# Kernel optimization log

Hardware: AMD Instinct MI355X
Metric: run time of the kernel (lower is better)

Reference implementation:

```python
import jax, jax.numpy as jnp
import numpy as np
from jax import lax

HIDDEN_CH = 32
KS = 3


def _conv(x, w):
    # x: [B, Cin, H, W], w: [Cout, Cin, k, k] -> [B, Cout, H, W] (SAME padding)
    return lax.conv_general_dilated(
        x, w, window_strides=(1, 1), padding='SAME',
        dimension_numbers=('NCHW', 'OIHW', 'NCHW'))


def _cell(x, h, gw, gb, cw, cb):
    combined = jnp.concatenate([x, h], axis=1)
    gates = jax.nn.sigmoid(_conv(combined, gw) + gb[None, :, None, None])
    r, z = jnp.split(gates, 2, axis=1)
    combined_r = jnp.concatenate([x, r * h], axis=1)
    n = jnp.tanh(_conv(combined_r, cw) + cb[None, :, None, None])
    return (1.0 - z) * h + z * n


def setup_inputs() -> dict:
    key = jax.random.key(0)
    ks = jax.random.split(key, 9)
    B, T, H, W = 8, 16, 128, 128
    hc = HIDDEN_CH
    seq = jax.random.normal(ks[0], (B, T, H, W), dtype=jnp.float32)

    def conv_init(k, cout, cin):
        fan_in = cin * KS * KS
        bound = 1.0 / np.sqrt(fan_in)
        return jax.random.uniform(k, (cout, cin, KS, KS), jnp.float32, -bound, bound)

    def bias_init(k, cout, cin):
        bound = 1.0 / np.sqrt(cin * KS * KS)
        return jax.random.uniform(k, (cout,), jnp.float32, -bound, bound)

    # Layer 0: input_ch=1, layer 1: input_ch=hc
    gw0 = conv_init(ks[1], 2 * hc, 1 + hc)
    gb0 = bias_init(ks[2], 2 * hc, 1 + hc)
    cw0 = conv_init(ks[3], hc, 1 + hc)
    cb0 = bias_init(ks[4], hc, 1 + hc)
    gw1 = conv_init(ks[5], 2 * hc, hc + hc)
    gb1 = bias_init(ks[6], 2 * hc, hc + hc)
    cw1 = conv_init(ks[7], hc, hc + hc)
    cb1 = bias_init(ks[8], hc, hc + hc)
    return {'seq': seq, 'gw0': gw0, 'gb0': gb0, 'cw0': cw0, 'cb0': cb0,
            'gw1': gw1, 'gb1': gb1, 'cw1': cw1, 'cb1': cb1}


def reference(seq, gw0, gb0, cw0, cb0, gw1, gb1, cw1, cb1):
    B, T, H, W = seq.shape
    hc = HIDDEN_CH
    h0 = jnp.zeros((B, hc, H, W), dtype=seq.dtype)
    h1 = jnp.zeros((B, hc, H, W), dtype=seq.dtype)
    # xs: [T, B, 1, H, W]
    xs = jnp.transpose(seq, (1, 0, 2, 3))[:, :, None, :, :]

    def step(carry, x_t):
        h0, h1 = carry
        h0 = _cell(x_t, h0, gw0, gb0, cw0, cb0)
        h1 = _cell(h0, h1, gw1, gb1, cw1, cb1)
        return (h0, h1), None

    (h0, h1), _ = lax.scan(step, (h0, h1), xs)
    return h1
```

## Files before the change

kernel.cpp:

```cpp
#include <hip/hip_runtime.h>


#define HH 128
#define PH 130
#define HW 16384
#define BB 8
#define TT 16

typedef _Float16 f16x8 __attribute__((ext_vector_type(8)));
typedef float f32x4 __attribute__((ext_vector_type(4)));
typedef unsigned int u32x4 __attribute__((ext_vector_type(4)));

__device__ __forceinline__ unsigned short f2h(float x){
    return __builtin_bit_cast(unsigned short, (_Float16)x);
}
__device__ __forceinline__ float h2f(unsigned short u){
    return (float)__builtin_bit_cast(_Float16, u);
}
__device__ __forceinline__ f16x8 ld_frag(const unsigned short* p){
    u32x4 v = *(const u32x4*)p;
    return __builtin_bit_cast(f16x8, v);
}
__device__ __forceinline__ f16x8 lds_frag_w(const unsigned short* base, int spix, int q){
    u32x4 v = *(const u32x4*)(base + spix * 32 + q * 8);
    return __builtin_bit_cast(f16x8, v);
}
__device__ __forceinline__ float sigmoid_f(float a){ return 1.0f / (1.0f + __expf(-a)); }
__device__ __forceinline__ float tanh_f(float a){ float e2 = __expf(2.0f * a); return 1.0f - 2.0f / (e2 + 1.0f); }

__device__ __forceinline__ void halo_rc(int s, int& gr, int& gc){
    s = s > 75 ? 75 : s;
    if (s < 34)      { gr = 0;            gc = s;      }
    else if (s < 68) { gr = 5;            gc = s - 34; }
    else if (s < 72) { gr = 1 + (s - 68); gc = 0;      }
    else             { gr = 1 + (s - 72); gc = 33;     }
}

__device__ __forceinline__ f16x8 x_im2col(const float* xt, int gr, int gc, int q){
    f16x8 v;
#pragma unroll
    for (int j = 0; j < 8; ++j) {
        int k = q * 8 + j;
        float f = 0.0f;
        if (k < 9) f = xt[(gr + k / 3) * 37 + gc + k % 3];
        v[j] = (_Float16)f;
    }
    return v;
}

__device__ __forceinline__ void stage_plane(unsigned short* slot,
    const unsigned short* __restrict__ g, int b, int prow0, int pcol0)
{
    const int wv = threadIdx.x >> 6, lane = threadIdx.x & 63;
    for (int k = wv; k < 18; k += 4) {
        int chunk = k * 64 + lane;
        int pix = chunk >> 2, part = chunk & 3;
        int r = pix / 36, c = pix - r * 36;
        int pr = prow0 + r; pr = pr < 0 ? 0 : (pr > 129 ? 129 : pr);
        int pc = pcol0 + c; pc = pc < 0 ? 0 : (pc > 129 ? 129 : pc);
        const unsigned short* ga = g + ((long)((b * PH + pr) * PH + pc) * 32 + part * 8);
        __builtin_amdgcn_global_load_lds(
            (const __attribute__((address_space(1))) unsigned int*)ga,
            (__attribute__((address_space(3))) unsigned int*)(slot + k * 512),
            16, 0, 0);
    }
}

__device__ __forceinline__ void stage_x(float* xt, const float* __restrict__ x,
                                        int irow0, int icol0)
{
    for (int p = threadIdx.x; p < 288; p += 256) {
        int r = p / 36, c = p - r * 36;
        int ir = irow0 + r, ic = icol0 + c;
        float v = 0.0f;
        if (ir >= 0 && ir < HH && ic >= 0 && ic < HH) v = x[ir * HH + ic];
        xt[r * 37 + c] = v;
    }
}

__global__ void prep_w(const float* __restrict__ w, unsigned short* __restrict__ wf,
                       int CO, int CIT, int NSTEP, int xmode)
{
    int idx = blockIdx.x * 256 + threadIdx.x;
    int total = NSTEP * CO * 32;
    if (idx >= total) return;
    int kk = idx & 31;
    int t  = idx >> 5;
    int co = t % CO;
    int s  = t / CO;
    float v = 0.0f;
    if (xmode && s == NSTEP - 1) {
        if (kk < 9) v = w[(co * CIT + 0) * 9 + kk];
    } else {
        int tap = s % 9;
        int cin = (s / 9) * 32 + kk + (xmode ? 1 : 0);
        v = w[(co * CIT + cin) * 9 + tap];
    }
    wf[idx] = f2h(v);
}

template<int L>
__global__ __launch_bounds__(256, (L == 0) ? 4 : 3)
void cell_fused(const unsigned short* __restrict__ Hin,
                unsigned short* __restrict__ Hout,
                const unsigned short* __restrict__ Xin,
                const float* __restrict__ xraw, long xbs,
                const unsigned short* __restrict__ Wg, const float* __restrict__ bg,
                const unsigned short* __restrict__ Wc, const float* __restrict__ bc)
{
    constexpr int NSLOT = (L == 0) ? 1 : 2;
    constexpr int KG = (L == 0) ? 10 : 18;
    constexpr int KC = (L == 0) ? 10 : 18;

    __shared__ __align__(16) unsigned short hsbuf[NSLOT][9216];
    __shared__ __align__(16) unsigned short rh[6528];
    __shared__ float xt[(L == 0) ? 296 : 1];

    unsigned short* hs0 = hsbuf[0];
    unsigned short* hs1 = hsbuf[NSLOT - 1];

    const int b  = blockIdx.y;
    const int tc = blockIdx.x & 3;
    const int tr = blockIdx.x >> 2;
    const int R0 = tr * 4, C0 = tc * 32;
    const int prow0 = R0 - 1, pcol0 = C0 - 1;

    if (L == 0) {
        stage_plane(hs0, Hin, b, prow0, pcol0);
        stage_x(xt, xraw + (long)b * xbs, R0 - 2, C0 - 2);
    } else {
        stage_plane(hs0, Xin, b, prow0, pcol0);
        stage_plane(hs1, Hin, b, prow0, pcol0);
    }
    __syncthreads();

    const int wv = threadIdx.x >> 6, lane = threadIdx.x & 63;
    const int m16 = lane & 15, q = lane >> 4;
    const unsigned short* hp = (L == 0) ? hs0 : hs1;

    int hr0, hc0, hr1, hc1;
    halo_rc(wv * 16 + m16, hr0, hc0);
    halo_rc(64 + m16, hr1, hc1);
    const bool HAS2 = (wv == 0);

    f32x4 gI[2][4];
    f32x4 gH[2][2];
#pragma unroll
    for (int ng = 0; ng < 4; ++ng) {
        float bv = bg[ng * 16 + m16];
#pragma unroll
        for (int mg = 0; mg < 2; ++mg) gI[mg][ng] = f32x4{bv, bv, bv, bv};
        if (ng < 2) { gH[0][ng] = f32x4{bv, bv, bv, bv}; gH[1][ng] = f32x4{bv, bv, bv, bv}; }
    }

#pragma unroll
    for (int s = 0; s < KG; ++s) {
        f16x8 Bf[4];
#pragma unroll
        for (int ng = 0; ng < 4; ++ng)
            Bf[ng] = ld_frag(Wg + (s * 64 + ng * 16 + m16) * 32 + q * 8);
        f16x8 AI[2], AH0, AH1;
        if (L == 0 && s == 9) {
#pragma unroll
            for (int mg = 0; mg < 2; ++mg)
                AI[mg] = x_im2col(xt, wv + 1, mg * 16 + 1 + m16, q);
            AH0 = x_im2col(xt, hr0, hc0, q);
            if (HAS2) AH1 = x_im2col(xt, hr1, hc1, q);
        } else {
            const int tap = (L == 0) ? s : (s % 9);
            const unsigned short* pl = (L == 1 && s >= 9) ? hs1 : hs0;
#pragma unroll
            for (int mg = 0; mg < 2; ++mg)
                AI[mg] = lds_frag_w(pl, (wv + 1 + tap / 3) * 36 + mg * 16 + 1 + m16 + tap % 3, q);
            AH0 = lds_frag_w(pl, (hr0 + tap / 3) * 36 + hc0 + tap % 3, q);
            if (HAS2) AH1 = lds_frag_w(pl, (hr1 + tap / 3) * 36 + hc1 + tap % 3, q);
        }
#pragma unroll
        for (int mg = 0; mg < 2; ++mg)
#pragma unroll
            for (int ng = 0; ng < 4; ++ng)
                gI[mg][ng] = __builtin_amdgcn_mfma_f32_16x16x32_f16(AI[mg], Bf[ng], gI[mg][ng], 0, 0, 0);
#pragma unroll
        for (int ng = 0; ng < 2; ++ng)
            gH[0][ng] = __builtin_amdgcn_mfma_f32_16x16x32_f16(AH0, Bf[ng], gH[0][ng], 0, 0, 0);
        if (HAS2) {
#pragma unroll
            for (int ng = 0; ng < 2; ++ng)
                gH[1][ng] = __builtin_amdgcn_mfma_f32_16x16x32_f16(AH1, Bf[ng], gH[1][ng], 0, 0, 0);
        }
    }

    unsigned int zpk[2][4];
#pragma unroll
    for (int mg = 0; mg < 2; ++mg)
#pragma unroll
        for (int rg = 0; rg < 4; ++rg) {
            int gr = wv + 1, gc = mg * 16 + 1 + q * 4 + rg;
            zpk[mg][rg] = (unsigned int)f2h(sigmoid_f(gI[mg][2][rg]))
                        | ((unsigned int)f2h(sigmoid_f(gI[mg][3][rg])) << 16);
#pragma unroll
            for (int ng = 0; ng < 2; ++ng) {
                int n = ng * 16 + m16;
                float rv = sigmoid_f(gI[mg][ng][rg]);
                float hv = h2f(hp[((gr + 1) * 36 + gc + 1) * 32 + n]);
                rh[(gr * 34 + gc) * 32 + n] = f2h(rv * hv);
            }
        }
#pragma unroll
    for (int rg = 0; rg < 4; ++rg) {
        int gr, gc; halo_rc(wv * 16 + q * 4 + rg, gr, gc);
#pragma unroll
        for (int ng = 0; ng < 2; ++ng) {
            int n = ng * 16 + m16;
            float rv = sigmoid_f(gH[0][ng][rg]);
            float hv = h2f(hp[((gr + 1) * 36 + gc + 1) * 32 + n]);
            rh[(gr * 34 + gc) * 32 + n] = f2h(rv * hv);
        }
    }
    if (HAS2) {
#pragma unroll
        for (int rg = 0; rg < 4; ++rg) {
            int gr, gc; halo_rc(64 + q * 4 + rg, gr, gc);
#pragma unroll
            for (int ng = 0; ng < 2; ++ng) {
                int n = ng * 16 + m16;
                float rv = sigmoid_f(gH[1][ng][rg]);
                float hv = h2f(hp[((gr + 1) * 36 + gc + 1) * 32 + n]);
                rh[(gr * 34 + gc) * 32 + n] = f2h(rv * hv);
            }
        }
    }
    __syncthreads();

    f32x4 cacc[2][2];
#pragma unroll
    for (int mg = 0; mg < 2; ++mg)
#pragma unroll
        for (int ng = 0; ng < 2; ++ng) {
            float bv = bc[ng * 16 + m16];
            cacc[mg][ng] = f32x4{bv, bv, bv, bv};
        }
#pragma unroll
    for (int s = 0; s < KC; ++s) {
        f16x8 Bf[2];
#pragma unroll
        for (int ng = 0; ng < 2; ++ng)
            Bf[ng] = ld_frag(Wc + (s * 32 + ng * 16 + m16) * 32 + q * 8);
        f16x8 A2[2];
        if (L == 0 && s == 9) {
#pragma unroll
            for (int mg = 0; mg < 2; ++mg)
                A2[mg] = x_im2col(xt, wv + 1, mg * 16 + 1 + m16, q);
        } else if (L == 1 && s < 9) {
#pragma unroll
            for (int mg = 0; mg < 2; ++mg)
                A2[mg] = lds_frag_w(hs0, (wv + 1 + s / 3) * 36 + mg * 16 + m16 + 1 + s % 3, q);
        } else {
            const int tap = (L == 0) ? s : (s - 9);
#pragma unroll
            for (int mg = 0; mg < 2; ++mg)
                A2[mg] = lds_frag_w(rh, (wv + tap / 3) * 34 + mg * 16 + m16 + tap % 3, q);
        }
#pragma unroll
        for (int mg = 0; mg < 2; ++mg)
#pragma unroll
            for (int ng = 0; ng < 2; ++ng)
                cacc[mg][ng] = __builtin_amdgcn_mfma_f32_16x16x32_f16(A2[mg], Bf[ng], cacc[mg][ng], 0, 0, 0);
    }
#pragma unroll
    for (int mg = 0; mg < 2; ++mg)
#pragma unroll
        for (int ng = 0; ng < 2; ++ng)
#pragma unroll
            for (int rg = 0; rg < 4; ++rg) {
                int lcol = mg * 16 + q * 4 + rg;
                int n = ng * 16 + m16;
                float nv = tanh_f(cacc[mg][ng][rg]);
                float zz = h2f((unsigned short)(zpk[mg][rg] >> (ng * 16)));
                float ho = h2f(hp[((wv + 2) * 36 + lcol + 2) * 32 + n]);
                long psp = (long)(b * PH + R0 + wv + 1) * PH + (C0 + lcol + 1);
                Hout[psp * 32 + n] = f2h((1.0f - zz) * ho + zz * nv);
            }
}

__global__ void final_out(const unsigned short* __restrict__ S1, float* __restrict__ out)
{
    int i = blockIdx.x * 256 + threadIdx.x;
    if (i >= BB * 32 * HW) return;
    int pix = i & 16383;
    int t = i >> 14;
    int c = t & 31, b = t >> 5;
    int r = pix >> 7, cc = pix & 127;
    long ps = (long)(b * PH + r + 1) * PH + cc + 1;
    out[i] = h2f(S1[ps * 32 + c]);
}

extern "C" void kernel_launch(void* const* d_in, const int* in_sizes, int n_in,
                              void* d_out, int out_size, void* d_ws, size_t ws_size,
                              hipStream_t stream)
{
    const float* seq = (const float*)d_in[0];
    const float* gw0 = (const float*)d_in[1];
    const float* gb0 = (const float*)d_in[2];
    const float* cw0 = (const float*)d_in[3];
    const float* cb0 = (const float*)d_in[4];
    const float* gw1 = (const float*)d_in[5];
    const float* gb1 = (const float*)d_in[6];
    const float* cw1 = (const float*)d_in[7];
    const float* cb1 = (const float*)d_in[8];
    float* out = (float*)d_out;

    const size_t NSP = (size_t)BB * PH * PH * 32;

    char* p = (char*)d_ws;
    unsigned short* S0A = (unsigned short*)p; p += NSP * 2;
    unsigned short* S0B = (unsigned short*)p; p += NSP * 2;
    unsigned short* S1A = (unsigned short*)p; p += NSP * 2;
    unsigned short* S1B = (unsigned short*)p; p += NSP * 2;
    unsigned short* WG0 = (unsigned short*)p; p += 20480 * 2;
    unsigned short* WC0 = (unsigned short*)p; p += 10240 * 2;
    unsigned short* WG1 = (unsigned short*)p; p += 36864 * 2;
    unsigned short* WC1 = (unsigned short*)p; p += 18432 * 2;

    hipMemsetAsync(S0A, 0, 4 * NSP * 2, stream);

    prep_w<<<(10 * 64 * 32 + 255) / 256, 256, 0, stream>>>(gw0, WG0, 64, 33, 10, 1);
    prep_w<<<(10 * 32 * 32 + 255) / 256, 256, 0, stream>>>(cw0, WC0, 32, 33, 10, 1);
    prep_w<<<(18 * 64 * 32 + 255) / 256, 256, 0, stream>>>(gw1, WG1, 64, 64, 18, 0);
    prep_w<<<(18 * 32 * 32 + 255) / 256, 256, 0, stream>>>(cw1, WC1, 32, 64, 18, 0);

    dim3 grid(128, BB), block(256);
    const long xbs = (long)TT * HW;
    unsigned short *s0r = S0A, *s0w = S0B, *s1r = S1A, *s1w = S1B;
    for (int t = 0; t < TT; ++t) {
        const float* xt = seq + (long)t * HW;
        cell_fused<0><<<grid, block, 0, stream>>>(s0r, s0w, (const unsigned short*)0,
                                                  xt, xbs, WG0, gb0, WC0, cb0);
        cell_fused<1><<<grid, block, 0, stream>>>(s1r, s1w, s0w,
                                                  (const float*)0, xbs, WG1, gb1, WC1, cb1);
        unsigned short* tmp;
        tmp = s0r; s0r = s0w; s0w = tmp;
        tmp = s1r; s1r = s1w; s1w = tmp;
    }
    final_out<<<(BB * 32 * HW + 255) / 256, 256, 0, stream>>>(s1r, out);
}
```

Baseline: 1.189 ms.

## Fuse all timesteps into one persistent cooperative kernel with larger tiles

Replaces the 32 per-layer, per-timestep launches with a single cooperative persistent kernel that uses grid-wide syncs between layer steps. The tile grows from 4x32 to 8x32 pixels with 512 threads, which shrinks the share of halo recompute. The final layer writes fp32 output directly through an LDS transpose, removing the separate final_out pass, and the x input is read straight from seq. In exchange it relies on 512 blocks being co-resident and on grid-sync cost, with a non-cooperative multi-launch fallback if the cooperative launch fails.

```diff
diff --git a/kernel.cpp b/kernel.cpp
--- a/kernel.cpp
+++ b/kernel.cpp
@@ -1,4 +1,5 @@
 #include <hip/hip_runtime.h>
+#include <hip/hip_cooperative_groups.h>
 
 
 #define HH 128
@@ -7,6 +8,8 @@
 #define BB 8
 #define TT 16
 
+namespace cg = cooperative_groups;
+
 typedef _Float16 f16x8 __attribute__((ext_vector_type(8)));
 typedef float f32x4 __attribute__((ext_vector_type(4)));
 typedef unsigned int u32x4 __attribute__((ext_vector_type(4)));
@@ -28,12 +31,18 @@
 __device__ __forceinline__ float sigmoid_f(float a){ return 1.0f / (1.0f + __expf(-a)); }
 __device__ __forceinline__ float tanh_f(float a){ float e2 = __expf(2.0f * a); return 1.0f - 2.0f / (e2 + 1.0f); }
 
-__device__ __forceinline__ void halo_rc(int s, int& gr, int& gc){
-    s = s > 75 ? 75 : s;
+struct SmemT {
+    unsigned short hs[2][13824];
+    unsigned short rh[10880];
+    float xt[444];
+};
+
+__device__ __forceinline__ void halo_rc10(int s, int& gr, int& gc){
+    s = s > 83 ? 83 : s;
     if (s < 34)      { gr = 0;            gc = s;      }
-    else if (s < 68) { gr = 5;            gc = s - 34; }
-    else if (s < 72) { gr = 1 + (s - 68); gc = 0;      }
-    else             { gr = 1 + (s - 72); gc = 33;     }
+    else if (s < 68) { gr = 9;            gc = s - 34; }
+    else if (s < 76) { gr = 1 + (s - 68); gc = 0;      }
+    else             { gr = 1 + (s - 76); gc = 33;     }
 }
 
 __device__ __forceinline__ f16x8 x_im2col(const float* xt, int gr, int gc, int q){
@@ -48,33 +57,21 @@
     return v;
 }
 
-__device__ __forceinline__ void stage_plane(unsigned short* slot,
-    const unsigned short* __restrict__ g, int b, int prow0, int pcol0)
+__device__ __forceinline__ void stage_plane12(unsigned short* slot,
+    const unsigned short* __restrict__ g, int b, int pr0, int pc0)
 {
     const int wv = threadIdx.x >> 6, lane = threadIdx.x & 63;
-    for (int k = wv; k < 18; k += 4) {
+    for (int k = wv; k < 27; k += 8) {
         int chunk = k * 64 + lane;
         int pix = chunk >> 2, part = chunk & 3;
         int r = pix / 36, c = pix - r * 36;
-        int pr = prow0 + r; pr = pr < 0 ? 0 : (pr > 129 ? 129 : pr);
-        int pc = pcol0 + c; pc = pc < 0 ? 0 : (pc > 129 ? 129 : pc);
+        int pr = pr0 + r; pr = pr < 0 ? 0 : (pr > 129 ? 129 : pr);
+        int pc = pc0 + c; pc = pc < 0 ? 0 : (pc > 129 ? 129 : pc);
         const unsigned short* ga = g + ((long)((b * PH + pr) * PH + pc) * 32 + part * 8);
         __builtin_amdgcn_global_load_lds(
             (const __attribute__((address_space(1))) unsigned int*)ga,
             (__attribute__((address_space(3))) unsigned int*)(slot + k * 512),
             16, 0, 0);
-    }
-}
-
-__device__ __forceinline__ void stage_x(float* xt, const float* __restrict__ x,
-                                        int irow0, int icol0)
-{
-    for (int p = threadIdx.x; p < 288; p += 256) {
-        int r = p / 36, c = p - r * 36;
-        int ir = irow0 + r, ic = icol0 + c;
-        float v = 0.0f;
-        if (ir >= 0 && ir < HH && ic >= 0 && ic < HH) v = x[ir * HH + ic];
-        xt[r * 37 + c] = v;
     }
 }
 
@@ -99,58 +96,52 @@
     wf[idx] = f2h(v);
 }
 
-template<int L>
-__global__ __launch_bounds__(256, (L == 0) ? 4 : 3)
-void cell_fused(const unsigned short* __restrict__ Hin,
-                unsigned short* __restrict__ Hout,
-                const unsigned short* __restrict__ Xin,
-                const float* __restrict__ xraw, long xbs,
-                const unsigned short* __restrict__ Wg, const float* __restrict__ bg,
-                const unsigned short* __restrict__ Wc, const float* __restrict__ bc)
-{
-    constexpr int NSLOT = (L == 0) ? 1 : 2;
+template<int L, int EMIT>
+__device__ __forceinline__ void do_cell(SmemT& sm,
+    const unsigned short* __restrict__ Hin,
+    unsigned short* __restrict__ Hout,
+    const unsigned short* __restrict__ Xin,
+    const float* __restrict__ seq, int t,
+    const unsigned short* __restrict__ Wg, const float* __restrict__ bg,
+    const unsigned short* __restrict__ Wc, const float* __restrict__ bc,
+    float* __restrict__ out, int b, int R0, int C0)
+{
     constexpr int KG = (L == 0) ? 10 : 18;
     constexpr int KC = (L == 0) ? 10 : 18;
 
-    __shared__ __align__(16) unsigned short hsbuf[NSLOT][9216];
-    __shared__ __align__(16) unsigned short rh[6528];
-    __shared__ float xt[(L == 0) ? 296 : 1];
-
-    unsigned short* hs0 = hsbuf[0];
-    unsigned short* hs1 = hsbuf[NSLOT - 1];
-
-    const int b  = blockIdx.y;
-    const int tc = blockIdx.x & 3;
-    const int tr = blockIdx.x >> 2;
-    const int R0 = tr * 4, C0 = tc * 32;
-    const int prow0 = R0 - 1, pcol0 = C0 - 1;
-
     if (L == 0) {
-        stage_plane(hs0, Hin, b, prow0, pcol0);
-        stage_x(xt, xraw + (long)b * xbs, R0 - 2, C0 - 2);
+        stage_plane12(sm.hs[0], Hin, b, R0 - 1, C0 - 1);
+        if (threadIdx.x < 444) {
+            int p = threadIdx.x;
+            int r = p / 37, c = p - r * 37;
+            int ir = R0 - 2 + r, ic = C0 - 2 + c;
+            float v = 0.0f;
+            if (ir >= 0 && ir < HH && ic >= 0 && ic < HH)
+                v = seq[((long)b * TT + t) * HW + ir * HH + ic];
+            sm.xt[p] = v;
+        }
     } else {
-        stage_plane(hs0, Xin, b, prow0, pcol0);
-        stage_plane(hs1, Hin, b, prow0, pcol0);
+        stage_plane12(sm.hs[0], Xin, b, R0 - 1, C0 - 1);
+        stage_plane12(sm.hs[1], Hin, b, R0 - 1, C0 - 1);
     }
     __syncthreads();
 
     const int wv = threadIdx.x >> 6, lane = threadIdx.x & 63;
     const int m16 = lane & 15, q = lane >> 4;
-    const unsigned short* hp = (L == 0) ? hs0 : hs1;
-
-    int hr0, hc0, hr1, hc1;
-    halo_rc(wv * 16 + m16, hr0, hc0);
-    halo_rc(64 + m16, hr1, hc1);
-    const bool HAS2 = (wv == 0);
+    const unsigned short* hp = (L == 0) ? sm.hs[0] : sm.hs[1];
+
+    const bool HASH = (wv >= 2);
+    int hgr = 0, hgc = 0;
+    halo_rc10((wv - 2) * 16 + m16, hgr, hgc);
 
     f32x4 gI[2][4];
-    f32x4 gH[2][2];
+    f32x4 gH[2];
 #pragma unroll
     for (int ng = 0; ng < 4; ++ng) {
         float bv = bg[ng * 16 + m16];
 #pragma unroll
         for (int mg = 0; mg < 2; ++mg) gI[mg][ng] = f32x4{bv, bv, bv, bv};
-        if (ng < 2) { gH[0][ng] = f32x4{bv, bv, bv, bv}; gH[1][ng] = f32x4{bv, bv, bv, bv}; }
+        if (ng < 2) gH[ng] = f32x4{bv, bv, bv, bv};
     }
 
 #pragma unroll
@@ -159,34 +150,29 @@
 #pragma unroll
         for (int ng = 0; ng < 4; ++ng)
             Bf[ng] = ld_frag(Wg + (s * 64 + ng * 16 + m16) * 32 + q * 8);
-        f16x8 AI[2], AH0, AH1;
+        f16x8 AI[2], AH;
         if (L == 0 && s == 9) {
 #pragma unroll
             for (int mg = 0; mg < 2; ++mg)
-                AI[mg] = x_im2col(xt, wv + 1, mg * 16 + 1 + m16, q);
-            AH0 = x_im2col(xt, hr0, hc0, q);
-            if (HAS2) AH1 = x_im2col(xt, hr1, hc1, q);
+                AI[mg] = x_im2col(sm.xt, wv + 1, mg * 16 + 1 + m16, q);
+            AH = x_im2col(sm.xt, hgr, hgc, q);
         } else {
             const int tap = (L == 0) ? s : (s % 9);
-            const unsigned short* pl = (L == 1 && s >= 9) ? hs1 : hs0;
+            const unsigned short* pl = (L == 1 && s >= 9) ? sm.hs[1] : sm.hs[0];
 #pragma unroll
             for (int mg = 0; mg < 2; ++mg)
                 AI[mg] = lds_frag_w(pl, (wv + 1 + tap / 3) * 36 + mg * 16 + 1 + m16 + tap % 3, q);
-            AH0 = lds_frag_w(pl, (hr0 + tap / 3) * 36 + hc0 + tap % 3, q);
-            if (HAS2) AH1 = lds_frag_w(pl, (hr1 + tap / 3) * 36 + hc1 + tap % 3, q);
+            AH = lds_frag_w(pl, (hgr + tap / 3) * 36 + hgc + tap % 3, q);
         }
 #pragma unroll
         for (int mg = 0; mg < 2; ++mg)
 #pragma unroll
             for (int ng = 0; ng < 4; ++ng)
                 gI[mg][ng] = __builtin_amdgcn_mfma_f32_16x16x32_f16(AI[mg], Bf[ng], gI[mg][ng], 0, 0, 0);
-#pragma unroll
-        for (int ng = 0; ng < 2; ++ng)
-            gH[0][ng] = __builtin_amdgcn_mfma_f32_16x16x32_f16(AH0, Bf[ng], gH[0][ng], 0, 0, 0);
-        if (HAS2) {
+        if (HASH) {
 #pragma unroll
             for (int ng = 0; ng < 2; ++ng)
-                gH[1][ng] = __builtin_amdgcn_mfma_f32_16x16x32_f16(AH1, Bf[ng], gH[1][ng], 0, 0, 0);
+                gH[ng] = __builtin_amdgcn_mfma_f32_16x16x32_f16(AH, Bf[ng], gH[ng], 0, 0, 0);
         }
     }
 
@@ -203,30 +189,19 @@
                 int n = ng * 16 + m16;
                 float rv = sigmoid_f(gI[mg][ng][rg]);
                 float hv = h2f(hp[((gr + 1) * 36 + gc + 1) * 32 + n]);
-                rh[(gr * 34 + gc) * 32 + n] = f2h(rv * hv);
+                sm.rh[(gr * 34 + gc) * 32 + n] = f2h(rv * hv);
             }
         }
-#pragma unroll
-    for (int rg = 0; rg < 4; ++rg) {
-        int gr, gc; halo_rc(wv * 16 + q * 4 + rg, gr, gc);
-#pragma unroll
-        for (int ng = 0; ng < 2; ++ng) {
-            int n = ng * 16 + m16;
-            float rv = sigmoid_f(gH[0][ng][rg]);
-            float hv = h2f(hp[((gr + 1) * 36 + gc + 1) * 32 + n]);
-            rh[(gr * 34 + gc) * 32 + n] = f2h(rv * hv);
-        }
-    }
-    if (HAS2) {
+    if (HASH) {
 #pragma unroll
         for (int rg = 0; rg < 4; ++rg) {
-            int gr, gc; halo_rc(64 + q * 4 + rg, gr, gc);
+            int gr, gc; halo_rc10((wv - 2) * 16 + q * 4 + rg, gr, gc);
 #pragma unroll
             for (int ng = 0; ng < 2; ++ng) {
                 int n = ng * 16 + m16;
-                float rv = sigmoid_f(gH[1][ng][rg]);
+                float rv = sigmoid_f(gH[ng][rg]);
                 float hv = h2f(hp[((gr + 1) * 36 + gc + 1) * 32 + n]);
-                rh[(gr * 34 + gc) * 32 + n] = f2h(rv * hv);
+                sm.rh[(gr * 34 + gc) * 32 + n] = f2h(rv * hv);
             }
         }
     }
@@ -250,16 +225,16 @@
         if (L == 0 && s == 9) {
 #pragma unroll
             for (int mg = 0; mg < 2; ++mg)
-                A2[mg] = x_im2col(xt, wv + 1, mg * 16 + 1 + m16, q);
+                A2[mg] = x_im2col(sm.xt, wv + 1, mg * 16 + 1 + m16, q);
         } else if (L == 1 && s < 9) {
 #pragma unroll
             for (int mg = 0; mg < 2; ++mg)
-                A2[mg] = lds_frag_w(hs0, (wv + 1 + s / 3) * 36 + mg * 16 + m16 + 1 + s % 3, q);
+                A2[mg] = lds_frag_w(sm.hs[0], (wv + 1 + s / 3) * 36 + mg * 16 + m16 + 1 + s % 3, q);
         } else {
             const int tap = (L == 0) ? s : (s - 9);
 #pragma unroll
             for (int mg = 0; mg < 2; ++mg)
-                A2[mg] = lds_frag_w(rh, (wv + tap / 3) * 34 + mg * 16 + m16 + tap % 3, q);
+                A2[mg] = lds_frag_w(sm.rh, (wv + tap / 3) * 34 + mg * 16 + m16 + tap % 3, q);
         }
 #pragma unroll
         for (int mg = 0; mg < 2; ++mg)
@@ -267,6 +242,8 @@
             for (int ng = 0; ng < 2; ++ng)
                 cacc[mg][ng] = __builtin_amdgcn_mfma_f32_16x16x32_f16(A2[mg], Bf[ng], cacc[mg][ng], 0, 0, 0);
     }
+
+    unsigned short hvout[2][2][4];
 #pragma unroll
     for (int mg = 0; mg < 2; ++mg)
 #pragma unroll
@@ -278,21 +255,85 @@
                 float nv = tanh_f(cacc[mg][ng][rg]);
                 float zz = h2f((unsigned short)(zpk[mg][rg] >> (ng * 16)));
                 float ho = h2f(hp[((wv + 2) * 36 + lcol + 2) * 32 + n]);
-                long psp = (long)(b * PH + R0 + wv + 1) * PH + (C0 + lcol + 1);
-                Hout[psp * 32 + n] = f2h((1.0f - zz) * ho + zz * nv);
+                float hnew = (1.0f - zz) * ho + zz * nv;
+                if (!EMIT) {
+                    long psp = (long)(b * PH + R0 + wv + 1) * PH + (C0 + lcol + 1);
+                    Hout[psp * 32 + n] = f2h(hnew);
+                } else {
+                    hvout[mg][ng][rg] = f2h(hnew);
+                }
             }
-}
-
-__global__ void final_out(const unsigned short* __restrict__ S1, float* __restrict__ out)
-{
-    int i = blockIdx.x * 256 + threadIdx.x;
-    if (i >= BB * 32 * HW) return;
-    int pix = i & 16383;
-    int t = i >> 14;
-    int c = t & 31, b = t >> 5;
-    int r = pix >> 7, cc = pix & 127;
-    long ps = (long)(b * PH + r + 1) * PH + cc + 1;
-    out[i] = h2f(S1[ps * 32 + c]);
+
+    if (EMIT) {
+        __syncthreads();
+        unsigned short* scr = sm.rh;
+#pragma unroll
+        for (int mg = 0; mg < 2; ++mg)
+#pragma unroll
+            for (int ng = 0; ng < 2; ++ng)
+#pragma unroll
+                for (int rg = 0; rg < 4; ++rg)
+                    scr[((wv * 32 + mg * 16 + q * 4 + rg) * 32) + ng * 16 + m16] = hvout[mg][ng][rg];
+        __syncthreads();
+        const int tid = threadIdx.x;
+        const int rowid = tid >> 1, half = tid & 1;
+        const int n = rowid >> 3, wr = rowid & 7;
+        long obase = ((long)(b * 32 + n) * HH + (R0 + wr)) * HH + C0 + half * 16;
+#pragma unroll
+        for (int j = 0; j < 16; ++j)
+            out[obase + j] = h2f(scr[(wr * 32 + half * 16 + j) * 32 + n]);
+    }
+}
+
+__global__ __launch_bounds__(512, 4)
+void gru_persistent(unsigned short* S0A, unsigned short* S0B,
+                    unsigned short* S1A, unsigned short* S1B,
+                    const float* seq,
+                    const unsigned short* WG0, const float* gb0,
+                    const unsigned short* WC0, const float* cb0,
+                    const unsigned short* WG1, const float* gb1,
+                    const unsigned short* WC1, const float* cb1,
+                    float* out)
+{
+    __shared__ __align__(16) SmemT sm;
+    cg::grid_group gg = cg::this_grid();
+    const int wg = blockIdx.x;
+    const int b = wg >> 6, tr = (wg >> 2) & 15, tc = wg & 3;
+    const int R0 = tr * 8, C0 = tc * 32;
+    unsigned short *h0r = S0A, *h0w = S0B, *h1r = S1A, *h1w = S1B;
+    for (int t = 0; t < TT; ++t) {
+        do_cell<0, 0>(sm, h0r, h0w, (const unsigned short*)0, seq, t,
+                      WG0, gb0, WC0, cb0, (float*)0, b, R0, C0);
+        gg.sync();
+        if (t == TT - 1) {
+            do_cell<1, 1>(sm, h1r, h1w, h0w, seq, t,
+                          WG1, gb1, WC1, cb1, out, b, R0, C0);
+        } else {
+            do_cell<1, 0>(sm, h1r, h1w, h0w, seq, t,
+                          WG1, gb1, WC1, cb1, (float*)0, b, R0, C0);
+            gg.sync();
+        }
+        unsigned short* tmp;
+        tmp = h0r; h0r = h0w; h0w = tmp;
+        tmp = h1r; h1r = h1w; h1w = tmp;
+    }
+}
+
+template<int L, int EMIT>
+__global__ __launch_bounds__(512, 4)
+void gru_step(const unsigned short* __restrict__ Hin,
+              unsigned short* __restrict__ Hout,
+              const unsigned short* __restrict__ Xin,
+              const float* __restrict__ seq, int t,
+              const unsigned short* __restrict__ Wg, const float* __restrict__ bg,
+              const unsigned short* __restrict__ Wc, const float* __restrict__ bc,
+              float* __restrict__ out)
+{
+    __shared__ __align__(16) SmemT sm;
+    const int wg = blockIdx.x;
+    const int b = wg >> 6, tr = (wg >> 2) & 15, tc = wg & 3;
+    do_cell<L, EMIT>(sm, Hin, Hout, Xin, seq, t, Wg, bg, Wc, bc, out,
+                     b, tr * 8, tc * 32);
 }
 
 extern "C" void kernel_launch(void* const* d_in, const int* in_sizes, int n_in,
@@ -329,18 +370,28 @@
     prep_w<<<(18 * 64 * 32 + 255) / 256, 256, 0, stream>>>(gw1, WG1, 64, 64, 18, 0);
     prep_w<<<(18 * 32 * 32 + 255) / 256, 256, 0, stream>>>(cw1, WC1, 32, 64, 18, 0);
 
-    dim3 grid(128, BB), block(256);
-    const long xbs = (long)TT * HW;
-    unsigned short *s0r = S0A, *s0w = S0B, *s1r = S1A, *s1w = S1B;
-    for (int t = 0; t < TT; ++t) {
-        const float* xt = seq + (long)t * HW;
-        cell_fused<0><<<grid, block, 0, stream>>>(s0r, s0w, (const unsigned short*)0,
-                                                  xt, xbs, WG0, gb0, WC0, cb0);
-        cell_fused<1><<<grid, block, 0, stream>>>(s1r, s1w, s0w,
-                                                  (const float*)0, xbs, WG1, gb1, WC1, cb1);
-        unsigned short* tmp;
-        tmp = s0r; s0r = s0w; s0w = tmp;
-        tmp = s1r; s1r = s1w; s1w = tmp;
-    }
-    final_out<<<(BB * 32 * HW + 255) / 256, 256, 0, stream>>>(s1r, out);
-}
+    void* ka[] = {
+        (void*)&S0A, (void*)&S0B, (void*)&S1A, (void*)&S1B, (void*)&seq,
+        (void*)&WG0, (void*)&gb0, (void*)&WC0, (void*)&cb0,
+        (void*)&WG1, (void*)&gb1, (void*)&WC1, (void*)&cb1, (void*)&out
+    };
+    hipError_t e = hipLaunchCooperativeKernel((const void*)gru_persistent,
+                                              dim3(512), dim3(512), ka, 0, stream);
+    if (e != hipSuccess) {
+        (void)hipGetLastError();
+        unsigned short *h0r = S0A, *h0w = S0B, *h1r = S1A, *h1w = S1B;
+        for (int t = 0; t < TT; ++t) {
+            gru_step<0, 0><<<dim3(512), dim3(512), 0, stream>>>(
+                h0r, h0w, (const unsigned short*)0, seq, t, WG0, gb0, WC0, cb0, (float*)0);
+            if (t == TT - 1)
+                gru_step<1, 1><<<dim3(512), dim3(512), 0, stream>>>(
+                    h1r, h1w, h0w, seq, t, WG1, gb1, WC1, cb1, out);
+            else
+                gru_step<1, 0><<<dim3(512), dim3(512), 0, stream>>>(
+                    h1r, h1w, h0w, seq, t, WG1, gb1, WC1, cb1, (float*)0);
+            unsigned short* tmp;
+            tmp = h0r; h0r = h0w; h0w = tmp;
+            tmp = h1r; h1r = h1w; h1w = tmp;
+        }
+    }
+}
```

After: 4.724 ms. 3.97x slower.

## Wavefront-schedule layer0 step t+1 with layer1 step t in one launch

Applied to the files above, without the earlier changes.

Restructures the time loop so each launch runs layer-1 at step t and layer-0 at step t+1 together, as two halves of a grid with blockIdx.z. The two cells are independent, so this halves the number of serialized launches and lets both layers fill the GPU at once. The final layer-1 cell writes the fp32 NCHW output directly through an LDS transpose, removing the separate final_out kernel. In exchange, layer-0 blocks now run under the layer-1 occupancy bound of 3 and reserve the larger shared memory footprint.

```diff
diff --git a/kernel.cpp b/kernel.cpp
--- a/kernel.cpp
+++ b/kernel.cpp
@@ -63,18 +63,6 @@
             (const __attribute__((address_space(1))) unsigned int*)ga,
             (__attribute__((address_space(3))) unsigned int*)(slot + k * 512),
             16, 0, 0);
-    }
-}
-
-__device__ __forceinline__ void stage_x(float* xt, const float* __restrict__ x,
-                                        int irow0, int icol0)
-{
-    for (int p = threadIdx.x; p < 288; p += 256) {
-        int r = p / 36, c = p - r * 36;
-        int ir = irow0 + r, ic = icol0 + c;
-        float v = 0.0f;
-        if (ir >= 0 && ir < HH && ic >= 0 && ic < HH) v = x[ir * HH + ic];
-        xt[r * 37 + c] = v;
     }
 }
 
@@ -99,35 +87,31 @@
     wf[idx] = f2h(v);
 }
 
-template<int L>
-__global__ __launch_bounds__(256, (L == 0) ? 4 : 3)
-void cell_fused(const unsigned short* __restrict__ Hin,
-                unsigned short* __restrict__ Hout,
-                const unsigned short* __restrict__ Xin,
-                const float* __restrict__ xraw, long xbs,
-                const unsigned short* __restrict__ Wg, const float* __restrict__ bg,
-                const unsigned short* __restrict__ Wc, const float* __restrict__ bc)
-{
-    constexpr int NSLOT = (L == 0) ? 1 : 2;
+template<int L, int EMIT>
+__device__ __forceinline__ void do_cell(
+    unsigned short* hs0, unsigned short* hs1, unsigned short* rh, float* xt,
+    const unsigned short* __restrict__ Hin,
+    unsigned short* __restrict__ Hout,
+    const unsigned short* __restrict__ Xin,
+    const float* __restrict__ seq, int t,
+    const unsigned short* __restrict__ Wg, const float* __restrict__ bg,
+    const unsigned short* __restrict__ Wc, const float* __restrict__ bc,
+    float* __restrict__ out, int b, int R0, int C0)
+{
     constexpr int KG = (L == 0) ? 10 : 18;
     constexpr int KC = (L == 0) ? 10 : 18;
-
-    __shared__ __align__(16) unsigned short hsbuf[NSLOT][9216];
-    __shared__ __align__(16) unsigned short rh[6528];
-    __shared__ float xt[(L == 0) ? 296 : 1];
-
-    unsigned short* hs0 = hsbuf[0];
-    unsigned short* hs1 = hsbuf[NSLOT - 1];
-
-    const int b  = blockIdx.y;
-    const int tc = blockIdx.x & 3;
-    const int tr = blockIdx.x >> 2;
-    const int R0 = tr * 4, C0 = tc * 32;
     const int prow0 = R0 - 1, pcol0 = C0 - 1;
 
     if (L == 0) {
         stage_plane(hs0, Hin, b, prow0, pcol0);
-        stage_x(xt, xraw + (long)b * xbs, R0 - 2, C0 - 2);
+        const float* x = seq + ((long)b * TT + t) * HW;
+        for (int p = threadIdx.x; p < 288; p += 256) {
+            int r = p / 36, c = p - r * 36;
+            int ir = R0 - 2 + r, ic = C0 - 2 + c;
+            float v = 0.0f;
+            if (ir >= 0 && ir < HH && ic >= 0 && ic < HH) v = x[ir * HH + ic];
+            xt[r * 37 + c] = v;
+        }
     } else {
         stage_plane(hs0, Xin, b, prow0, pcol0);
         stage_plane(hs1, Hin, b, prow0, pcol0);
@@ -267,6 +251,8 @@
             for (int ng = 0; ng < 2; ++ng)
                 cacc[mg][ng] = __builtin_amdgcn_mfma_f32_16x16x32_f16(A2[mg], Bf[ng], cacc[mg][ng], 0, 0, 0);
     }
+
+    unsigned short hvout[2][2][4];
 #pragma unroll
     for (int mg = 0; mg < 2; ++mg)
 #pragma unroll
@@ -278,21 +264,85 @@
                 float nv = tanh_f(cacc[mg][ng][rg]);
                 float zz = h2f((unsigned short)(zpk[mg][rg] >> (ng * 16)));
                 float ho = h2f(hp[((wv + 2) * 36 + lcol + 2) * 32 + n]);
-                long psp = (long)(b * PH + R0 + wv + 1) * PH + (C0 + lcol + 1);
-                Hout[psp * 32 + n] = f2h((1.0f - zz) * ho + zz * nv);
+                float hnew = (1.0f - zz) * ho + zz * nv;
+                if (!EMIT) {
+                    long psp = (long)(b * PH + R0 + wv + 1) * PH + (C0 + lcol + 1);
+                    Hout[psp * 32 + n] = f2h(hnew);
+                } else {
+                    hvout[mg][ng][rg] = f2h(hnew);
+                }
             }
-}
-
-__global__ void final_out(const unsigned short* __restrict__ S1, float* __restrict__ out)
-{
-    int i = blockIdx.x * 256 + threadIdx.x;
-    if (i >= BB * 32 * HW) return;
-    int pix = i & 16383;
-    int t = i >> 14;
-    int c = t & 31, b = t >> 5;
-    int r = pix >> 7, cc = pix & 127;
-    long ps = (long)(b * PH + r + 1) * PH + cc + 1;
-    out[i] = h2f(S1[ps * 32 + c]);
+
+    if (EMIT) {
+        __syncthreads();
+        unsigned short* scr = rh;
+#pragma unroll
+        for (int mg = 0; mg < 2; ++mg)
+#pragma unroll
+            for (int ng = 0; ng < 2; ++ng)
+#pragma unroll
+                for (int rg = 0; rg < 4; ++rg)
+                    scr[((wv * 32 + mg * 16 + q * 4 + rg) * 32) + ng * 16 + m16] = hvout[mg][ng][rg];
+        __syncthreads();
+        const int tid = threadIdx.x;
+        const int rowid = tid >> 1, half = tid & 1;
+        const int c = rowid >> 2, wr = rowid & 3;
+        long obase = ((long)(b * 32 + c) * HH + (R0 + wr)) * HH + C0 + half * 16;
+#pragma unroll
+        for (int j = 0; j < 16; ++j)
+            out[obase + j] = h2f(scr[(wr * 32 + half * 16 + j) * 32 + c]);
+    }
+}
+
+
+__global__ __launch_bounds__(256, 4)
+void cell_l0(const unsigned short* __restrict__ Hin, unsigned short* __restrict__ Hout,
+             const float* __restrict__ seq, int t,
+             const unsigned short* __restrict__ Wg, const float* __restrict__ bg,
+             const unsigned short* __restrict__ Wc, const float* __restrict__ bc)
+{
+    __shared__ __align__(16) unsigned short hs0[9216];
+    __shared__ __align__(16) unsigned short rh[6528];
+    __shared__ float xt[304];
+    const int b = blockIdx.y, tc = blockIdx.x & 3, tr = blockIdx.x >> 2;
+    do_cell<0, 0>(hs0, hs0, rh, xt, Hin, Hout, (const unsigned short*)0,
+                  seq, t, Wg, bg, Wc, bc, (float*)0, b, tr * 4, tc * 32);
+}
+
+__global__ __launch_bounds__(256, 3)
+void step_pair(const unsigned short* __restrict__ h1r, unsigned short* __restrict__ h1w,
+               const unsigned short* __restrict__ h0r, unsigned short* __restrict__ h0w,
+               const float* __restrict__ seq, int tnext,
+               const unsigned short* __restrict__ WG0, const float* __restrict__ gb0,
+               const unsigned short* __restrict__ WC0, const float* __restrict__ cb0,
+               const unsigned short* __restrict__ WG1, const float* __restrict__ gb1,
+               const unsigned short* __restrict__ WC1, const float* __restrict__ cb1)
+{
+    __shared__ __align__(16) unsigned short hs[2][9216];
+    __shared__ __align__(16) unsigned short rh[6528];
+    __shared__ float xt[304];
+    const int b = blockIdx.y, tc = blockIdx.x & 3, tr = blockIdx.x >> 2;
+    if (blockIdx.z == 0)
+        do_cell<1, 0>(hs[0], hs[1], rh, xt, h1r, h1w, h0r,
+                      seq, 0, WG1, gb1, WC1, cb1, (float*)0, b, tr * 4, tc * 32);
+    else
+        do_cell<0, 0>(hs[0], hs[1], rh, xt, h0r, h0w, (const unsigned short*)0,
+                      seq, tnext, WG0, gb0, WC0, cb0, (float*)0, b, tr * 4, tc * 32);
+}
+
+__global__ __launch_bounds__(256, 3)
+void cell_l1_emit(const unsigned short* __restrict__ Hin,
+                  const unsigned short* __restrict__ Xin,
+                  const unsigned short* __restrict__ Wg, const float* __restrict__ bg,
+                  const unsigned short* __restrict__ Wc, const float* __restrict__ bc,
+                  float* __restrict__ out)
+{
+    __shared__ __align__(16) unsigned short hs[2][9216];
+    __shared__ __align__(16) unsigned short rh[6528];
+    __shared__ float xt[4];
+    const int b = blockIdx.y, tc = blockIdx.x & 3, tr = blockIdx.x >> 2;
+    do_cell<1, 1>(hs[0], hs[1], rh, xt, Hin, (unsigned short*)0, Xin,
+                  (const float*)0, 0, Wg, bg, Wc, bc, out, b, tr * 4, tc * 32);
 }
 
 extern "C" void kernel_launch(void* const* d_in, const int* in_sizes, int n_in,
@@ -329,18 +379,18 @@
     prep_w<<<(18 * 64 * 32 + 255) / 256, 256, 0, stream>>>(gw1, WG1, 64, 64, 18, 0);
     prep_w<<<(18 * 32 * 32 + 255) / 256, 256, 0, stream>>>(cw1, WC1, 32, 64, 18, 0);
 
-    dim3 grid(128, BB), block(256);
-    const long xbs = (long)TT * HW;
-    unsigned short *s0r = S0A, *s0w = S0B, *s1r = S1A, *s1w = S1B;
-    for (int t = 0; t < TT; ++t) {
-        const float* xt = seq + (long)t * HW;
-        cell_fused<0><<<grid, block, 0, stream>>>(s0r, s0w, (const unsigned short*)0,
-                                                  xt, xbs, WG0, gb0, WC0, cb0);
-        cell_fused<1><<<grid, block, 0, stream>>>(s1r, s1w, s0w,
-                                                  (const float*)0, xbs, WG1, gb1, WC1, cb1);
+    dim3 grid1(128, BB, 1), grid2(128, BB, 2), block(256);
+
+    cell_l0<<<grid1, block, 0, stream>>>(S0A, S0B, seq, 0, WG0, gb0, WC0, cb0);
+
+    unsigned short *h0r = S0B, *h0w = S0A, *h1r = S1A, *h1w = S1B;
+    for (int t = 0; t < TT - 1; ++t) {
+        step_pair<<<grid2, block, 0, stream>>>(h1r, h1w, h0r, h0w, seq, t + 1,
+                                               WG0, gb0, WC0, cb0,
+                                               WG1, gb1, WC1, cb1);
         unsigned short* tmp;
-        tmp = s0r; s0r = s0w; s0w = tmp;
-        tmp = s1r; s1r = s1w; s1w = tmp;
-    }
-    final_out<<<(BB * 32 * HW + 255) / 256, 256, 0, stream>>>(s1r, out);
-}
+        tmp = h0r; h0r = h0w; h0w = tmp;
+        tmp = h1r; h1r = h1w; h1w = tmp;
+    }
+    cell_l1_emit<<<grid1, block, 0, stream>>>(h1r, h0r, WG1, gb1, WC1, cb1, out);
+}
```

After: 1.087 ms. 1.09x faster.
